# Kernel optimization log

Hardware: AMD Instinct MI355X
Metric: run time of the kernel (lower is better)

## Reference

```python
import jax, jax.numpy as jnp
import numpy as np

B, S, D, H, V, C = 4, 2048, 1024, 16, 32000, 10
FFN_DIM = 2 * D
HD = D // H
SCALE = float(np.sqrt(HD))


def _posenc(seq, d):
    pos = jnp.arange(seq, dtype=jnp.float32)[:, None]
    div = jnp.exp(jnp.arange(0, d, 2, dtype=jnp.float32) * (-np.log(10000.0) / d))
    pe = jnp.zeros((seq, d), dtype=jnp.float32)
    pe = pe.at[:, 0::2].set(jnp.sin(pos * div))
    pe = pe.at[:, 1::2].set(jnp.cos(pos * div))
    return pe


def _layernorm(x, g, b, eps=1e-5):
    mu = jnp.mean(x, axis=-1, keepdims=True)
    var = jnp.mean(jnp.square(x - mu), axis=-1, keepdims=True)
    return (x - mu) * jax.lax.rsqrt(var + eps) * g + b


def setup_inputs() -> dict:
    key = jax.random.key(0)
    ks = jax.random.split(key, 10)
    x_ids = jax.random.randint(ks[0], (B, S), 0, V, dtype=jnp.int64 if jax.config.jax_enable_x64 else jnp.int32)
    mask = jnp.ones((B, S), dtype=jnp.int32)
    emb = (jax.random.normal(ks[1], (V, D), jnp.float32) * 0.02).at[0].set(0.0)  # padding_idx=0
    qkv_w = jax.random.normal(ks[2], (3 * D, D), jnp.float32) * 0.02
    fc_w = jax.random.normal(ks[3], (D, D), jnp.float32) * 0.02
    fc_b = jnp.zeros((D,), jnp.float32)
    ln1_g = jnp.ones((D,), jnp.float32); ln1_b = jnp.zeros((D,), jnp.float32)
    ffn_w1 = jax.random.normal(ks[4], (FFN_DIM, D), jnp.float32) * 0.02
    ffn_b1 = jnp.zeros((FFN_DIM,), jnp.float32)
    ffn_w2 = jax.random.normal(ks[5], (D, FFN_DIM), jnp.float32) * 0.02
    ffn_b2 = jnp.zeros((D,), jnp.float32)
    ln2_g = jnp.ones((D,), jnp.float32); ln2_b = jnp.zeros((D,), jnp.float32)
    pr_w1 = jax.random.normal(ks[6], (D, D), jnp.float32) * 0.02
    pr_b1 = jnp.zeros((D,), jnp.float32)
    pr_w2 = jax.random.normal(ks[7], (C, D), jnp.float32) * 0.02
    pr_b2 = jnp.zeros((C,), jnp.float32)
    return dict(x_ids=x_ids, mask=mask, emb=emb, qkv_w=qkv_w, fc_w=fc_w, fc_b=fc_b,
                ln1_g=ln1_g, ln1_b=ln1_b, ffn_w1=ffn_w1, ffn_b1=ffn_b1,
                ffn_w2=ffn_w2, ffn_b2=ffn_b2, ln2_g=ln2_g, ln2_b=ln2_b,
                pr_w1=pr_w1, pr_b1=pr_b1, pr_w2=pr_w2, pr_b2=pr_b2)


def reference(x_ids, mask, emb, qkv_w, fc_w, fc_b, ln1_g, ln1_b,
              ffn_w1, ffn_b1, ffn_w2, ffn_b2, ln2_g, ln2_b,
              pr_w1, pr_b1, pr_w2, pr_b2):
    # embedding + absolute positional encoding
    x = emb[x_ids] + _posenc(S, D)  # [B,S,D]
    residual = x
    # multi-head attention (dropout is identity at eval)
    qkv = jnp.einsum('bsd,ed->bse', x, qkv_w)  # [B,S,3D]
    q, k, v = jnp.split(qkv, 3, axis=-1)
    q = q.reshape(B, S, H, HD)
    k = k.reshape(B, S, H, HD)
    v = v.reshape(B, S, H, HD)
    attn = jnp.einsum('bqhd,bkhd->bhqk', q, k) / SCALE  # [B,H,S,S]
    attn = jnp.where(mask[:, None, None, :] == 0, -jnp.inf, attn)
    attn = jax.nn.softmax(attn, axis=-1)
    o = jnp.einsum('bhqk,bkhd->bqhd', attn, v).reshape(B, S, D)
    o = jnp.einsum('bsd,ed->bse', o, fc_w) + fc_b
    x = _layernorm(o + residual, ln1_g, ln1_b)
    # FFN block (residual + LayerNorm inside)
    h = jax.nn.gelu(jnp.einsum('bsd,fd->bsf', x, ffn_w1) + ffn_b1, approximate=False)
    h = jnp.einsum('bsf,df->bsd', h, ffn_w2) + ffn_b2
    x = _layernorm(h + x, ln2_g, ln2_b)
    # masked max-pool over sequence
    x = jnp.where(mask[:, :, None] == 0, -jnp.inf, x).max(axis=1)  # [B,D]
    # prediction head
    h = jax.nn.gelu(x @ pr_w1.T + pr_b1, approximate=False)
    logits = h @ pr_w2.T + pr_b2  # [B,C]
    return logits
```

## Files before the change

### kernel.cpp

```cpp
#include <hip/hip_runtime.h>
#include <math.h>

#define B_   4
#define S_   2048
#define D_   1024
#define H_   16
#define HD_  64
#define C_   10
#define FFN_ 2048
#define M_   (B_ * S_)
#define D3_  (3 * D_)

typedef unsigned short u16;
typedef __bf16 bf16x8 __attribute__((ext_vector_type(8)));
typedef float  f32x4  __attribute__((ext_vector_type(4)));

#define EXPSCL 0.18033688011112042f

__device__ __forceinline__ u16 f2bf(float f) {
  union { float f; unsigned u; } x; x.f = f;
  unsigned r = x.u + 0x7fffu + ((x.u >> 16) & 1u);
  return (u16)(r >> 16);
}
__device__ __forceinline__ unsigned pkbf(float a, float b) {
  union { float f; unsigned u; } x, y; x.f = a; y.f = b;
  return __builtin_amdgcn_perm(y.u + 0x8000u, x.u + 0x8000u, 0x07060302u);
}
__device__ __forceinline__ float gelu_f(float x) {
  return 0.5f * x * (1.f + erff(x * 0.70710678118654752440f));
}
__device__ __forceinline__ void gload_lds16(const void* g, void* l) {
  __builtin_amdgcn_global_load_lds(
      (const __attribute__((address_space(1))) unsigned int*)g,
      (__attribute__((address_space(3))) unsigned int*)l, 16, 0, 0);
}
__device__ __forceinline__ bf16x8 ldsfrag(const u16* buf, int rowbase, int fr, int kb) {
  return *(const bf16x8*)&buf[(rowbase + fr) * 64 + ((kb ^ (fr & 7)) << 3)];
}

#define CV0 786432
#define CV1 262144
#define CV2 524288
#define CV3 524288
__global__ __launch_bounds__(256) void cvt4_kernel(const float* __restrict__ s0,
                                                   const float* __restrict__ s1,
                                                   const float* __restrict__ s2,
                                                   const float* __restrict__ s3,
                                                   u16* __restrict__ d0,
                                                   u16* __restrict__ d1,
                                                   u16* __restrict__ d2,
                                                   u16* __restrict__ d3) {
  int v = blockIdx.x * 256 + threadIdx.x;
  const float* s; u16* d;
  if (v < CV0) { s = s0; d = d0; }
  else if (v < CV0 + CV1) { s = s1; d = d1; v -= CV0; }
  else if (v < CV0 + CV1 + CV2) { s = s2; d = d2; v -= CV0 + CV1; }
  else { s = s3; d = d3; v -= CV0 + CV1 + CV2; }
  const int i = v * 4;
  f32x4 x = *(const f32x4*)&s[i];
  ushort4 o;
  o.x = f2bf(x[0]); o.y = f2bf(x[1]); o.z = f2bf(x[2]); o.w = f2bf(x[3]);
  *(ushort4*)&d[i] = o;
}

__global__ __launch_bounds__(256) void embed_kernel(const int* __restrict__ ids,
                                                    const float* __restrict__ emb,
                                                    float* __restrict__ resid,
                                                    u16* __restrict__ xb) {
  const int m  = blockIdx.x;
  const int s  = m & (S_ - 1);
  const int id = ids[m];
  const int d0 = threadIdx.x * 4;
#pragma unroll
  for (int k = 0; k < 4; ++k) {
    const int d   = d0 + k;
    const float e = emb[(size_t)id * D_ + d];
    const float fr  = expf((float)(d & ~1) * (-9.210340371976184f / 1024.0f));
    const float ang = (float)s * fr;
    const float pe  = (d & 1) ? cosf(ang) : sinf(ang);
    const float v   = e + pe;
    resid[(size_t)m * D_ + d] = v;
    xb[(size_t)m * D_ + d]    = f2bf(v);
  }
}

template <int BIAS, int GELU, int OUTBF, int QSCALE>
__global__ __launch_bounds__(256) void gemm_bt(const u16* __restrict__ A,
                                               const u16* __restrict__ W,
                                               const float* __restrict__ bias,
                                               float* __restrict__ outf,
                                               u16* __restrict__ outb,
                                               int M, int N, int K) {
  __shared__ u16 As[128 * 64];
  __shared__ u16 Bs[128 * 64];
  const int tid  = threadIdx.x;
  const int lane = tid & 63;
  const int w    = tid >> 6;
  const int bx   = blockIdx.x, by = blockIdx.y;
  const int l3   = lane >> 3;
  const int sb   = (lane & 7) ^ l3;
  const u16* Ag0 = A + (size_t)(by * 128 + w * 32 + l3) * K + sb * 8;
  const u16* Wg0 = W + (size_t)(bx * 128 + w * 32 + l3) * K + sb * 8;

  f32x4 acc[4][4] = {};
  const int wr  = (w & 1) * 64;
  const int wc  = (w >> 1) * 64;
  const int fr  = lane & 15;
  const int fq  = lane >> 4;

  for (int kt = 0; kt < K; kt += 64) {
#pragma unroll
    for (int c = 0; c < 4; ++c) {
      gload_lds16(Ag0 + (size_t)(c * 8) * K + kt, &As[(w * 32 + c * 8) * 64]);
      gload_lds16(Wg0 + (size_t)(c * 8) * K + kt, &Bs[(w * 32 + c * 8) * 64]);
    }
    __syncthreads();
#pragma unroll
    for (int ks = 0; ks < 2; ++ks) {
      const int kb = ks * 4 + fq;
      bf16x8 af[4], bfr[4];
#pragma unroll
      for (int i = 0; i < 4; ++i) af[i] = ldsfrag(As, wr + i * 16, fr, kb);
#pragma unroll
      for (int j = 0; j < 4; ++j) bfr[j] = ldsfrag(Bs, wc + j * 16, fr, kb);
#pragma unroll
      for (int i = 0; i < 4; ++i)
#pragma unroll
        for (int j = 0; j < 4; ++j)
          acc[i][j] = __builtin_amdgcn_mfma_f32_16x16x32_bf16(bfr[j], af[i], acc[i][j], 0, 0, 0);
    }
    __syncthreads();
  }

  const float qs = (QSCALE && bx < 8) ? EXPSCL : 1.f;
#pragma unroll
  for (int i = 0; i < 4; ++i) {
    const int m = by * 128 + wr + i * 16 + fr;
#pragma unroll
    for (int j = 0; j < 4; ++j) {
      const int nb = bx * 128 + wc + j * 16 + fq * 4;
      f32x4 v = acc[i][j];
      if (BIAS) v += *(const f32x4*)&bias[nb];
      if (GELU) {
        v[0] = gelu_f(v[0]); v[1] = gelu_f(v[1]);
        v[2] = gelu_f(v[2]); v[3] = gelu_f(v[3]);
      }
      if (QSCALE) v *= qs;
      if (OUTBF) {
        ushort4 pk;
        pk.x = f2bf(v[0]); pk.y = f2bf(v[1]); pk.z = f2bf(v[2]); pk.w = f2bf(v[3]);
        *(ushort4*)&outb[(size_t)m * N + nb] = pk;
      } else {
        *(f32x4*)&outf[(size_t)m * N + nb] = v;
      }
    }
  }
}

__global__ __launch_bounds__(256) void vtrans_kernel(const u16* __restrict__ qkv,
                                                     u16* __restrict__ vt) {
  __shared__ u16 t[64 * 65];
  const int tid = threadIdx.x;
  const int st = blockIdx.x, h = blockIdx.y, b = blockIdx.z;
  {
    const int r = tid & 63, cg = tid >> 6;
    const u16* src = qkv + (size_t)(b * S_ + st * 64 + r) * D3_ + 2 * D_ + h * 64 + cg * 16;
    union { uint4 q; u16 s[8]; } a, c;
    a.q = *(const uint4*)src;
    c.q = *(const uint4*)(src + 8);
    u16* dl = &t[r * 65 + cg * 16];
#pragma unroll
    for (int k = 0; k < 8; ++k) { dl[k] = a.s[k]; dl[8 + k] = c.s[k]; }
  }
  __syncthreads();
  const int d = tid >> 2, sq = tid & 3;
  union { uint4 q[2]; u16 s[16]; } o;
#pragma unroll
  for (int k = 0; k < 16; ++k) o.s[k] = t[(sq * 16 + k) * 65 + d];
  u16* dst = vt + ((size_t)((b * H_ + h) * 64 + d)) * S_ + st * 64 + sq * 16;
  *(uint4*)dst = o.q[0];
  *(uint4*)(dst + 8) = o.q[1];
}

__global__ __launch_bounds__(256) void attn_mfma_kernel(const u16* __restrict__ qkv,
                                                        const u16* __restrict__ vt,
                                                        const int* __restrict__ mask,
                                                        u16* __restrict__ attno) {
  __shared__ u16 Qs[128 * 64];
  __shared__ u16 Ks[64 * 64];
  __shared__ u16 Vts[64 * 64];
  __shared__ u16 Ps[4][32 * 64];
  __shared__ float mb[64];
  __shared__ int allv_s;
  const int tid = threadIdx.x, lane = tid & 63, w = tid >> 6;
  const int qt = blockIdx.x, h = blockIdx.y, b = blockIdx.z;
  const int l3 = lane >> 3;
  const int sb = (lane & 7) ^ l3;
  const int fr = lane & 15, fq = lane >> 4;

  {
    const u16* qbase = qkv + (size_t)(b * S_ + qt * 128 + w * 32) * D3_ + h * 64 + sb * 8;
#pragma unroll
    for (int c = 0; c < 4; ++c)
      gload_lds16(qbase + (size_t)(c * 8 + l3) * D3_, &Qs[(w * 32 + c * 8) * 64]);
  }
  if (tid == 0) allv_s = 1;
  __syncthreads();
  {
    int mv = 1;
#pragma unroll
    for (int s0 = 0; s0 < 8; ++s0) mv &= (mask[b * S_ + s0 * 256 + tid] != 0);
    if (__ballot(mv != 0) != ~0ull) {
      if (lane == 0) atomicAnd(&allv_s, 0);
    }
  }
  __syncthreads();
  const bool ALLV = (allv_s != 0);

  float l_st[2] = {0.f, 0.f};
  f32x4 ot[4][2] = {};
  u16* PsW = Ps[w];

  for (int kt = 0; kt < S_ / 64; ++kt) {
    __syncthreads();
    {
      const u16* kbase = qkv + (size_t)(b * S_ + kt * 64 + w * 16) * D3_ + D_ + h * 64 + sb * 8;
      gload_lds16(kbase + (size_t)l3 * D3_, &Ks[(w * 16) * 64]);
      gload_lds16(kbase + (size_t)(8 + l3) * D3_, &Ks[(w * 16 + 8) * 64]);
      const u16* vbase = vt + ((size_t)((b * H_ + h) * 64 + w * 16)) * S_ + kt * 64 + sb * 8;
      gload_lds16(vbase + (size_t)l3 * S_, &Vts[(w * 16) * 64]);
      gload_lds16(vbase + (size_t)(8 + l3) * S_, &Vts[(w * 16 + 8) * 64]);
    }
    if (!ALLV && tid < 64) mb[tid] = (mask[b * S_ + kt * 64 + tid] != 0) ? 0.f : -1e30f;
    __syncthreads();

    f32x4 sf[4][2] = {};
#pragma unroll
    for (int ks = 0; ks < 2; ++ks) {
      const int kb = ks * 4 + fq;
      bf16x8 qf0 = ldsfrag(Qs, w * 32, fr, kb);
      bf16x8 qf1 = ldsfrag(Qs, w * 32 + 16, fr, kb);
#pragma unroll
      for (int r4 = 0; r4 < 4; ++r4) {
        bf16x8 kf = ldsfrag(Ks, r4 * 16, fr, kb);
        sf[r4][0] = __builtin_amdgcn_mfma_f32_16x16x32_bf16(kf, qf0, sf[r4][0], 0, 0, 0);
        sf[r4][1] = __builtin_amdgcn_mfma_f32_16x16x32_bf16(kf, qf1, sf[r4][1], 0, 0, 0);
      }
    }
    if (!ALLV) {
#pragma unroll
      for (int r4 = 0; r4 < 4; ++r4) {
        const f32x4 vb = *(const f32x4*)&mb[r4 * 16 + fq * 4];
        sf[r4][0] += vb;
        sf[r4][1] += vb;
      }
    }

#pragma unroll
    for (int i = 0; i < 2; ++i) {
      const int prow = i * 16 + fr;
      u16* pw = PsW + prow * 64;
      float sum = l_st[i];
#pragma unroll
      for (int r4 = 0; r4 < 4; ++r4) {
        const float p0 = __builtin_exp2f(sf[r4][i][0]);
        const float p1 = __builtin_exp2f(sf[r4][i][1]);
        const float p2 = __builtin_exp2f(sf[r4][i][2]);
        const float p3 = __builtin_exp2f(sf[r4][i][3]);
        sum += (p0 + p1) + (p2 + p3);
        const int bk0 = 2 * r4 + (fq >> 1);
        const int off = ((bk0 ^ (prow & 7)) << 3) + ((fq & 1) << 2);
        uint2 pk; pk.x = pkbf(p0, p1); pk.y = pkbf(p2, p3);
        *(uint2*)&pw[off] = pk;
      }
      l_st[i] = sum;
    }
    asm volatile("s_waitcnt lgkmcnt(0)" ::: "memory");

#pragma unroll
    for (int ks = 0; ks < 2; ++ks) {
      const int kb = ks * 4 + fq;
      bf16x8 pf0 = ldsfrag(PsW, 0, fr, kb);
      bf16x8 pf1 = ldsfrag(PsW, 16, fr, kb);
#pragma unroll
      for (int db = 0; db < 4; ++db) {
        bf16x8 vf = ldsfrag(Vts, db * 16, fr, kb);
        ot[db][0] = __builtin_amdgcn_mfma_f32_16x16x32_bf16(vf, pf0, ot[db][0], 0, 0, 0);
        ot[db][1] = __builtin_amdgcn_mfma_f32_16x16x32_bf16(vf, pf1, ot[db][1], 0, 0, 0);
      }
    }
  }

#pragma unroll
  for (int i = 0; i < 2; ++i) {
    float l = l_st[i];
    l += __shfl_xor(l, 16);
    l += __shfl_xor(l, 32);
    const float inv = (l > 0.f) ? 1.f / l : 0.f;
    const int qrow = qt * 128 + w * 32 + i * 16 + fr;
    u16* dst = attno + (size_t)(b * S_ + qrow) * D_ + h * 64 + fq * 4;
#pragma unroll
    for (int db = 0; db < 4; ++db) {
      ushort4 pk;
      pk.x = f2bf(ot[db][i][0] * inv);
      pk.y = f2bf(ot[db][i][1] * inv);
      pk.z = f2bf(ot[db][i][2] * inv);
      pk.w = f2bf(ot[db][i][3] * inv);
      *(ushort4*)&dst[db * 16] = pk;
    }
  }
}

template <int WRITEB>
__global__ __launch_bounds__(256) void ln_kernel(const float* __restrict__ a,
                                                 const float* __restrict__ res,
                                                 const float* __restrict__ g,
                                                 const float* __restrict__ be,
                                                 float* __restrict__ outf,
                                                 u16* __restrict__ outb) {
  const int row = blockIdx.x, tid = threadIdx.x;
  const int lane = tid & 63, w = tid >> 6;
  const size_t base = (size_t)row * D_ + tid * 4;
  const f32x4 va = *(const f32x4*)(a + base);
  const f32x4 vr = *(const f32x4*)(res + base);
  const f32x4 v  = va + vr;
  float s = v[0] + v[1] + v[2] + v[3];
#pragma unroll
  for (int o = 32; o > 0; o >>= 1) s += __shfl_xor(s, o);
  __shared__ float red[8];
  if (lane == 0) red[w] = s;
  __syncthreads();
  const float mu = (red[0] + red[1] + red[2] + red[3]) * (1.f / D_);
  const f32x4 d = v - mu;
  float s2 = d[0] * d[0] + d[1] * d[1] + d[2] * d[2] + d[3] * d[3];
#pragma unroll
  for (int o = 32; o > 0; o >>= 1) s2 += __shfl_xor(s2, o);
  if (lane == 0) red[4 + w] = s2;
  __syncthreads();
  const float var = (red[4] + red[5] + red[6] + red[7]) * (1.f / D_);
  const float rs = rsqrtf(var + 1e-5f);
  f32x4 y;
#pragma unroll
  for (int k = 0; k < 4; ++k) {
    const int ch = tid * 4 + k;
    y[k] = d[k] * rs * g[ch] + be[ch];
  }
  *(f32x4*)&outf[base] = y;
  if (WRITEB) {
    ushort4 pk;
    pk.x = f2bf(y[0]); pk.y = f2bf(y[1]); pk.z = f2bf(y[2]); pk.w = f2bf(y[3]);
    *(ushort4*)&outb[base] = pk;
  }
}

__global__ __launch_bounds__(256) void pool_part_kernel(const float* __restrict__ x,
                                                        const int* __restrict__ mask,
                                                        float* __restrict__ part) {
  const int b = blockIdx.y, ch = blockIdx.x;
  const int d0 = threadIdx.x * 4;
  f32x4 acc = {-INFINITY, -INFINITY, -INFINITY, -INFINITY};
  for (int ss = 0; ss < 64; ++ss) {
    const int s = ch * 64 + ss;
    if (mask[b * S_ + s] != 0) {
      const f32x4 v = *(const f32x4*)&x[(size_t)(b * S_ + s) * D_ + d0];
      acc[0] = fmaxf(acc[0], v[0]);
      acc[1] = fmaxf(acc[1], v[1]);
      acc[2] = fmaxf(acc[2], v[2]);
      acc[3] = fmaxf(acc[3], v[3]);
    }
  }
  *(f32x4*)&part[(size_t)(b * 32 + ch) * D_ + d0] = acc;
}
__global__ __launch_bounds__(256) void pool_final_kernel(const float* __restrict__ part,
                                                         float* __restrict__ pooled) {
  const int b = blockIdx.x;
  const int d0 = threadIdx.x * 4;
  f32x4 acc = {-INFINITY, -INFINITY, -INFINITY, -INFINITY};
  for (int ch = 0; ch < 32; ++ch) {
    const f32x4 v = *(const f32x4*)&part[(size_t)(b * 32 + ch) * D_ + d0];
    acc[0] = fmaxf(acc[0], v[0]);
    acc[1] = fmaxf(acc[1], v[1]);
    acc[2] = fmaxf(acc[2], v[2]);
    acc[3] = fmaxf(acc[3], v[3]);
  }
  *(f32x4*)&pooled[(size_t)b * D_ + d0] = acc;
}

__global__ __launch_bounds__(256) void head1_kernel(const float* __restrict__ pooled,
                                                    const float* __restrict__ w,
                                                    const float* __restrict__ bias,
                                                    float* __restrict__ hh) {
  const int lane = threadIdx.x & 63;
  const int gw = blockIdx.x * 4 + (threadIdx.x >> 6);
  const int b = gw >> 10, n = gw & 1023;
  const float* p  = pooled + b * 1024;
  const float* wr = w + (size_t)n * 1024;
  float s = 0.f;
  for (int d = lane; d < 1024; d += 64) s += p[d] * wr[d];
#pragma unroll
  for (int off = 32; off > 0; off >>= 1) s += __shfl_xor(s, off);
  if (lane == 0) hh[b * 1024 + n] = gelu_f(s + bias[n]);
}
__global__ __launch_bounds__(256) void head2_kernel(const float* __restrict__ hh,
                                                    const float* __restrict__ w,
                                                    const float* __restrict__ bias,
                                                    float* __restrict__ out) {
  const int lane = threadIdx.x & 63;
  const int gw = blockIdx.x * 4 + (threadIdx.x >> 6);
  const int b = gw / 10, c = gw % 10;
  const float* p  = hh + b * 1024;
  const float* wr = w + (size_t)c * 1024;
  float s = 0.f;
  for (int d = lane; d < 1024; d += 64) s += p[d] * wr[d];
#pragma unroll
  for (int off = 32; off > 0; off >>= 1) s += __shfl_xor(s, off);
  if (lane == 0) out[b * 10 + c] = s + bias[c];
}

#define OFF_RESID  0UL
#define OFF_F1     33554432UL
#define OFF_XB     67108864UL
#define OFF_QKVB   83886080UL
#define OFF_ATTNO  134217728UL
#define OFF_WQKV   150994944UL
#define OFF_WFC    157286400UL
#define OFF_WF1    159383552UL
#define OFF_WF2    163577856UL
#define OFF_PART   167772160UL
#define OFF_POOLED 168296448UL
#define OFF_HH     168312832UL

extern "C" void kernel_launch(void* const* d_in, const int* in_sizes, int n_in,
                              void* d_out, int out_size, void* d_ws, size_t ws_size,
                              hipStream_t stream) {
  const int*   x_ids  = (const int*)d_in[0];
  const int*   mask   = (const int*)d_in[1];
  const float* emb    = (const float*)d_in[2];
  const float* qkv_w  = (const float*)d_in[3];
  const float* fc_w   = (const float*)d_in[4];
  const float* fc_b   = (const float*)d_in[5];
  const float* ln1_g  = (const float*)d_in[6];
  const float* ln1_b  = (const float*)d_in[7];
  const float* ffn_w1 = (const float*)d_in[8];
  const float* ffn_b1 = (const float*)d_in[9];
  const float* ffn_w2 = (const float*)d_in[10];
  const float* ffn_b2 = (const float*)d_in[11];
  const float* ln2_g  = (const float*)d_in[12];
  const float* ln2_b  = (const float*)d_in[13];
  const float* pr_w1  = (const float*)d_in[14];
  const float* pr_b1  = (const float*)d_in[15];
  const float* pr_w2  = (const float*)d_in[16];
  const float* pr_b2  = (const float*)d_in[17];
  float* out = (float*)d_out;
  char* ws = (char*)d_ws;

  float* resid  = (float*)(ws + OFF_RESID);
  float* f1     = (float*)(ws + OFF_F1);
  u16*   vtb    = (u16*)(ws + OFF_F1);
  u16*   xb     = (u16*)(ws + OFF_XB);
  u16*   qkvb   = (u16*)(ws + OFF_QKVB);
  u16*   hb     = (u16*)(ws + OFF_QKVB);
  u16*   attnob = (u16*)(ws + OFF_ATTNO);
  u16*   wqkvb  = (u16*)(ws + OFF_WQKV);
  u16*   wfcb   = (u16*)(ws + OFF_WFC);
  u16*   wf1b   = (u16*)(ws + OFF_WF1);
  u16*   wf2b   = (u16*)(ws + OFF_WF2);
  float* part   = (float*)(ws + OFF_PART);
  float* pooled = (float*)(ws + OFF_POOLED);
  float* hh     = (float*)(ws + OFF_HH);

  cvt4_kernel<<<8192, 256, 0, stream>>>(qkv_w, fc_w, ffn_w1, ffn_w2,
                                        wqkvb, wfcb, wf1b, wf2b);

  embed_kernel<<<M_, 256, 0, stream>>>(x_ids, emb, resid, xb);

  gemm_bt<0, 0, 1, 1><<<dim3(D3_ / 128, M_ / 128), 256, 0, stream>>>(
      xb, wqkvb, nullptr, nullptr, qkvb, M_, D3_, D_);

  vtrans_kernel<<<dim3(S_ / 64, H_, B_), 256, 0, stream>>>(qkvb, vtb);

  attn_mfma_kernel<<<dim3(S_ / 128, H_, B_), 256, 0, stream>>>(qkvb, vtb, mask, attnob);

  gemm_bt<1, 0, 0, 0><<<dim3(D_ / 128, M_ / 128), 256, 0, stream>>>(
      attnob, wfcb, fc_b, f1, nullptr, M_, D_, D_);

  ln_kernel<1><<<M_, 256, 0, stream>>>(f1, resid, ln1_g, ln1_b, resid, xb);

  gemm_bt<1, 1, 1, 0><<<dim3(FFN_ / 128, M_ / 128), 256, 0, stream>>>(
      xb, wf1b, ffn_b1, nullptr, hb, M_, FFN_, D_);

  gemm_bt<1, 0, 0, 0><<<dim3(D_ / 128, M_ / 128), 256, 0, stream>>>(
      hb, wf2b, ffn_b2, f1, nullptr, M_, D_, FFN_);

  ln_kernel<0><<<M_, 256, 0, stream>>>(f1, resid, ln2_g, ln2_b, f1, nullptr);

  pool_part_kernel<<<dim3(32, B_), 256, 0, stream>>>(f1, mask, part);
  pool_final_kernel<<<B_, 256, 0, stream>>>(part, pooled);

  head1_kernel<<<1024, 256, 0, stream>>>(pooled, pr_w1, pr_b1, hh);
  head2_kernel<<<10, 256, 0, stream>>>(hh, pr_w2, pr_b2, out);
}
```

Measured before the change: 636.2 us.

## Shrink attention LDS footprint and raise occupancy with per-half P staging

```diff
diff --git a/kernel.cpp b/kernel.cpp
--- a/kernel.cpp
+++ b/kernel.cpp
@@ -22,9 +22,10 @@
   unsigned r = x.u + 0x7fffu + ((x.u >> 16) & 1u);
   return (u16)(r >> 16);
 }
-__device__ __forceinline__ unsigned pkbf(float a, float b) {
-  union { float f; unsigned u; } x, y; x.f = a; y.f = b;
-  return __builtin_amdgcn_perm(y.u + 0x8000u, x.u + 0x8000u, 0x07060302u);
+__device__ __forceinline__ unsigned cvtpk(float lo, float hi) {
+  unsigned r;
+  asm("v_cvt_pk_bf16_f32 %0, %1, %2" : "=v"(r) : "v"(lo), "v"(hi));
+  return r;
 }
 __device__ __forceinline__ float gelu_f(float x) {
   return 0.5f * x * (1.f + erff(x * 0.70710678118654752440f));
@@ -182,16 +183,15 @@
   *(uint4*)(dst + 8) = o.q[1];
 }
 
-__global__ __launch_bounds__(256) void attn_mfma_kernel(const u16* __restrict__ qkv,
-                                                        const u16* __restrict__ vt,
-                                                        const int* __restrict__ mask,
-                                                        u16* __restrict__ attno) {
+__global__ __launch_bounds__(256, 4) void attn_mfma_kernel(const u16* __restrict__ qkv,
+                                                           const u16* __restrict__ vt,
+                                                           const int* __restrict__ mask,
+                                                           u16* __restrict__ attno) {
   __shared__ u16 Qs[128 * 64];
   __shared__ u16 Ks[64 * 64];
   __shared__ u16 Vts[64 * 64];
-  __shared__ u16 Ps[4][32 * 64];
-  __shared__ float mb[64];
-  __shared__ int allv_s;
+  __shared__ u16 Ps[4][16 * 64];
+  int* allv_p = (int*)&Ps[0][0];
   const int tid = threadIdx.x, lane = tid & 63, w = tid >> 6;
   const int qt = blockIdx.x, h = blockIdx.y, b = blockIdx.z;
   const int l3 = lane >> 3;
@@ -204,18 +204,18 @@
     for (int c = 0; c < 4; ++c)
       gload_lds16(qbase + (size_t)(c * 8 + l3) * D3_, &Qs[(w * 32 + c * 8) * 64]);
   }
-  if (tid == 0) allv_s = 1;
+  if (tid == 0) *allv_p = 1;
   __syncthreads();
   {
     int mv = 1;
 #pragma unroll
     for (int s0 = 0; s0 < 8; ++s0) mv &= (mask[b * S_ + s0 * 256 + tid] != 0);
     if (__ballot(mv != 0) != ~0ull) {
-      if (lane == 0) atomicAnd(&allv_s, 0);
+      if (lane == 0) atomicAnd(allv_p, 0);
     }
   }
   __syncthreads();
-  const bool ALLV = (allv_s != 0);
+  const bool ALLV = (*allv_p != 0);
 
   float l_st[2] = {0.f, 0.f};
   f32x4 ot[4][2] = {};
@@ -231,7 +231,6 @@
       gload_lds16(vbase + (size_t)l3 * S_, &Vts[(w * 16) * 64]);
       gload_lds16(vbase + (size_t)(8 + l3) * S_, &Vts[(w * 16 + 8) * 64]);
     }
-    if (!ALLV && tid < 64) mb[tid] = (mask[b * S_ + kt * 64 + tid] != 0) ? 0.f : -1e30f;
     __syncthreads();
 
     f32x4 sf[4][2] = {};
@@ -240,26 +239,39 @@
       const int kb = ks * 4 + fq;
       bf16x8 qf0 = ldsfrag(Qs, w * 32, fr, kb);
       bf16x8 qf1 = ldsfrag(Qs, w * 32 + 16, fr, kb);
+      __builtin_amdgcn_s_setprio(1);
 #pragma unroll
       for (int r4 = 0; r4 < 4; ++r4) {
         bf16x8 kf = ldsfrag(Ks, r4 * 16, fr, kb);
         sf[r4][0] = __builtin_amdgcn_mfma_f32_16x16x32_bf16(kf, qf0, sf[r4][0], 0, 0, 0);
         sf[r4][1] = __builtin_amdgcn_mfma_f32_16x16x32_bf16(kf, qf1, sf[r4][1], 0, 0, 0);
       }
+      __builtin_amdgcn_s_setprio(0);
     }
     if (!ALLV) {
 #pragma unroll
       for (int r4 = 0; r4 < 4; ++r4) {
-        const f32x4 vb = *(const f32x4*)&mb[r4 * 16 + fq * 4];
+        const int4 mm = *(const int4*)&mask[b * S_ + kt * 64 + r4 * 16 + fq * 4];
+        f32x4 vb;
+        vb[0] = mm.x ? 0.f : -1e30f;
+        vb[1] = mm.y ? 0.f : -1e30f;
+        vb[2] = mm.z ? 0.f : -1e30f;
+        vb[3] = mm.w ? 0.f : -1e30f;
         sf[r4][0] += vb;
         sf[r4][1] += vb;
       }
     }
 
+    bf16x8 vfc[2][4];
+#pragma unroll
+    for (int ks = 0; ks < 2; ++ks)
+#pragma unroll
+      for (int db = 0; db < 4; ++db)
+        vfc[ks][db] = ldsfrag(Vts, db * 16, fr, ks * 4 + fq);
+
 #pragma unroll
     for (int i = 0; i < 2; ++i) {
-      const int prow = i * 16 + fr;
-      u16* pw = PsW + prow * 64;
+      u16* pw = PsW + fr * 64;
       float sum = l_st[i];
 #pragma unroll
       for (int r4 = 0; r4 < 4; ++r4) {
@@ -269,25 +281,22 @@
         const float p3 = __builtin_exp2f(sf[r4][i][3]);
         sum += (p0 + p1) + (p2 + p3);
         const int bk0 = 2 * r4 + (fq >> 1);
-        const int off = ((bk0 ^ (prow & 7)) << 3) + ((fq & 1) << 2);
-        uint2 pk; pk.x = pkbf(p0, p1); pk.y = pkbf(p2, p3);
+        const int off = ((bk0 ^ (fr & 7)) << 3) + ((fq & 1) << 2);
+        uint2 pk; pk.x = cvtpk(p0, p1); pk.y = cvtpk(p2, p3);
         *(uint2*)&pw[off] = pk;
       }
       l_st[i] = sum;
-    }
-    asm volatile("s_waitcnt lgkmcnt(0)" ::: "memory");
-
-#pragma unroll
-    for (int ks = 0; ks < 2; ++ks) {
-      const int kb = ks * 4 + fq;
-      bf16x8 pf0 = ldsfrag(PsW, 0, fr, kb);
-      bf16x8 pf1 = ldsfrag(PsW, 16, fr, kb);
+      asm volatile("s_waitcnt lgkmcnt(0)" ::: "memory");
+
+      bf16x8 pf0 = ldsfrag(PsW, 0, fr, fq);
+      bf16x8 pf1 = ldsfrag(PsW, 0, fr, 4 + fq);
+      __builtin_amdgcn_s_setprio(1);
 #pragma unroll
       for (int db = 0; db < 4; ++db) {
-        bf16x8 vf = ldsfrag(Vts, db * 16, fr, kb);
-        ot[db][0] = __builtin_amdgcn_mfma_f32_16x16x32_bf16(vf, pf0, ot[db][0], 0, 0, 0);
-        ot[db][1] = __builtin_amdgcn_mfma_f32_16x16x32_bf16(vf, pf1, ot[db][1], 0, 0, 0);
+        ot[db][i] = __builtin_amdgcn_mfma_f32_16x16x32_bf16(vfc[0][db], pf0, ot[db][i], 0, 0, 0);
+        ot[db][i] = __builtin_amdgcn_mfma_f32_16x16x32_bf16(vfc[1][db], pf1, ot[db][i], 0, 0, 0);
       }
+      __builtin_amdgcn_s_setprio(0);
     }
   }
 
```

Measured after the change: 720.3 us. 1.13x slower.
